# Optimization experiments

Hardware: AMD Instinct MI355X
Metric: run time of the kernel (lower is better)

## Reference

```python
import jax, jax.numpy as jnp
import numpy as np

EPS = 1e-5

def mvn(x):
    # per-(N,C) spatial mean/std normalization; torch .var is unbiased (ddof=1)
    mean = jnp.mean(x, axis=(2, 3), keepdims=True)
    var = jnp.var(x, axis=(2, 3), ddof=1, keepdims=True)
    return (x - mean) / jnp.sqrt(var + EPS)

def conv1x1(x, w, b):
    # w: [O, C] (1x1 conv collapsed), x: [B, C, H, W]
    return jnp.einsum('bchw,oc->bohw', x, w) + b[None, :, None, None]

def conv3x3(x, w, b):
    # w: [O, I, 3, 3], VALID padding (snet uses padding=0)
    y = jax.lax.conv_general_dilated(x, w, (1, 1), 'VALID',
                                     dimension_numbers=('NCHW', 'OIHW', 'NCHW'))
    return y + b[None, :, None, None]

def safe_cbrt(x):
    # pow(relu(x), 1/3) with safe gradient at 0 (forward identical)
    pos = x > 0
    return jnp.where(pos, jnp.power(jnp.where(pos, x, 1.0), 1.0 / 3.0), 0.0)

def _forward(content, style, wf_san, bf_san, wg_san, bg_san, wh_san, bh_san,
             wf_mcc, bf_mcc, wg_mcc, bg_mcc, w_fc, b_fc, w_out, b_out,
             wc1, bc1, wc2, bc2, wc3, bc3, ws1, bs1, ws2, bs2, ws3, bs3,
             w_unc, b_unc):
    B, C, H, W = content.shape
    cn = mvn(content)
    sn = mvn(style)

    # --- MCC branch: channel correlation statistic of style ---
    F_Fc = conv1x1(cn, wf_mcc, bf_mcc)                      # [B,C,H,W]
    g = conv1x1(sn, wg_mcc, bg_mcc).reshape(B, C, H * W)    # [B,C,HW]
    FC_S = jnp.sum(g * g, axis=-1) / jnp.sum(g, axis=-1)    # [B,C]
    FC_S = FC_S @ w_fc.T + b_fc                             # Linear
    part1 = F_Fc * FC_S[:, :, None, None]

    # --- WCT-like covariance branch (compressed 32-dim space) ---
    Fs0 = style - jnp.mean(style, axis=(2, 3), keepdims=True)  # nor_mean
    fc_ = conv1x1(jax.nn.relu(conv1x1(jax.nn.relu(conv1x1(cn, wc1, bc1)), wc2, bc2)), wc3, bc3)  # [B,32,H,W]
    fs_ = conv1x1(jax.nn.relu(conv3x3(jax.nn.relu(conv3x3(Fs0, ws1, bs1)), ws2, bs2)), ws3, bs3)  # [B,32,H-4,W-4]
    cdim = fc_.shape[1]
    fs_flat = fs_.reshape(B, cdim, -1)                       # [B,32,hw_s]
    cov = jnp.einsum('bci,bdi->bcd', fs_flat, fs_flat) / fs_flat.shape[2]  # [B,32,32]
    out = jnp.einsum('bcd,bdi->bci', cov, fc_.reshape(B, cdim, H * W)).reshape(B, cdim, H, W)
    part2 = conv1x1(out, w_unc, b_unc)                       # [B,512,H,W]

    # --- SANet-style attention branch ---
    F_s = conv1x1(cn, wf_san, bf_san).reshape(B, C, H * W)
    G_s = conv1x1(sn, wg_san, bg_san).reshape(B, C, H * W)
    H_s = conv1x1(style, wh_san, bh_san).reshape(B, C, H * W)
    S = jax.nn.softmax(jnp.einsum('bci,bcj->bij', F_s, G_s), axis=-1)  # [B,HW,HW]
    part3 = jnp.einsum('bcj,bij->bci', H_s, S).reshape(B, C, H, W)

    p = safe_cbrt(jax.nn.relu(part1 * part2 * part3))
    return conv1x1(p, w_out, b_out) + content


def setup_inputs() -> dict:
    key = jax.random.key(0)
    B, C, H, W = 16, 512, 32, 32
    s = 0.02
    shapes = {
        'content': (B, C, H, W), 'style': (B, C, H, W),
        'wf_san': (C, C), 'bf_san': (C,), 'wg_san': (C, C), 'bg_san': (C,),
        'wh_san': (C, C), 'bh_san': (C,),
        'wf_mcc': (C, C), 'bf_mcc': (C,), 'wg_mcc': (C, C), 'bg_mcc': (C,),
        'w_fc': (C, C), 'b_fc': (C,), 'w_out': (C, C), 'b_out': (C,),
        'wc1': (256, 512), 'bc1': (256,), 'wc2': (128, 256), 'bc2': (128,),
        'wc3': (32, 128), 'bc3': (32,),
        'ws1': (256, 512, 3, 3), 'bs1': (256,), 'ws2': (128, 256, 3, 3), 'bs2': (128,),
        'ws3': (32, 128), 'bs3': (32,),
        'w_unc': (512, 32), 'b_unc': (512,),
    }
    d = {}
    for i, (name, shp) in enumerate(shapes.items()):
        k = jax.random.fold_in(key, i)
        scale = 1.0 if name in ('content', 'style') else s
        d[name] = jax.random.normal(k, shp, dtype=jnp.float32) * scale
    return d


def reference(content, style, wf_san, bf_san, wg_san, bg_san, wh_san, bh_san,
              wf_mcc, bf_mcc, wg_mcc, bg_mcc, w_fc, b_fc, w_out, b_out,
              wc1, bc1, wc2, bc2, wc3, bc3, ws1, bs1, ws2, bs2, ws3, bs3,
              w_unc, b_unc):
    return _forward(content, style, wf_san, bf_san, wg_san, bg_san, wh_san, bh_san,
                    wf_mcc, bf_mcc, wg_mcc, bg_mcc, w_fc, b_fc, w_out, b_out,
                    wc1, bc1, wc2, bc2, wc3, bc3, ws1, bs1, ws2, bs2, ws3, bs3,
                    w_unc, b_unc)
```

## Files before the change

kernel.cpp:

```cpp
#include <hip/hip_runtime.h>
#include <hip/hip_bf16.h>
#include <math.h>


typedef __attribute__((ext_vector_type(8))) short short8;
typedef __attribute__((ext_vector_type(4))) float f32x4;
typedef unsigned short us;
#define MFMA16 __builtin_amdgcn_mfma_f32_16x16x32_bf16

__device__ inline float b2f(us b) { return __uint_as_float(((unsigned)b) << 16); }
__device__ inline us f2b(float f) {
    unsigned u = __float_as_uint(f);
    return (us)((u + 0x7FFFu + ((u >> 16) & 1u)) >> 16);
}

__device__ inline double blockReduceSumD(double v, double* sh) {
    int t = threadIdx.x;
    sh[t] = v; __syncthreads();
    for (int s = blockDim.x >> 1; s > 0; s >>= 1) {
        if (t < s) sh[t] += sh[t + s];
        __syncthreads();
    }
    double r = sh[0]; __syncthreads();
    return r;
}

__global__ __launch_bounds__(256) void stats_k(const float* __restrict__ X,
                                               float* __restrict__ mean,
                                               float* __restrict__ inv, int HW) {
    __shared__ double sh[256];
    int bc = blockIdx.x;
    const float* x = X + (size_t)bc * HW;
    int t = threadIdx.x;
    float v[4];
    double s = 0.0;
    #pragma unroll
    for (int r = 0; r < 4; ++r) { v[r] = x[t + r * 256]; s += (double)v[r]; }
    double tot = blockReduceSumD(s, sh);
    double ss = 0.0;
    #pragma unroll
    for (int r = 0; r < 4; ++r) ss += (double)v[r] * (double)v[r];
    double tot2 = blockReduceSumD(ss, sh);
    if (t == 0) {
        double m = tot / HW;
        double var = (tot2 - tot * tot / HW) / (HW - 1);
        mean[bc] = (float)m;
        inv[bc] = (float)(1.0 / sqrt(var + 1e-5));
    }
}

__global__ __launch_bounds__(256) void trn_k(const float* __restrict__ X,
                                             const float* __restrict__ mean,
                                             const float* __restrict__ inv,
                                             us* __restrict__ Yn, us* __restrict__ Yc,
                                             us* __restrict__ Yr, int C, int HW) {
    __shared__ us Ln[64 * 65];
    __shared__ us Lc[64 * 65];
    __shared__ us Lr[64 * 65];
    int bz = blockIdx.z, c0 = blockIdx.y * 64, h0 = blockIdx.x * 64;
    const float* Xb = X + (size_t)bz * C * HW;
    int t = threadIdx.x;
    int cl = t >> 3, h8 = (t & 7) * 8;
    #pragma unroll
    for (int half = 0; half < 2; ++half) {
        int c = cl + half * 32;
        int gc = c0 + c;
        float m = mean[bz * C + gc], iv = inv[bz * C + gc];
        const float4* s4 = (const float4*)&Xb[(size_t)gc * HW + h0 + h8];
        float4 f0 = s4[0], f1 = s4[1];
        float vv[8] = {f0.x, f0.y, f0.z, f0.w, f1.x, f1.y, f1.z, f1.w};
        #pragma unroll
        for (int i = 0; i < 8; ++i) {
            int li = c * 65 + h8 + i;
            if (Yn) Ln[li] = f2b((vv[i] - m) * iv);
            if (Yc) Lc[li] = f2b(vv[i] - m);
            if (Yr) Lr[li] = f2b(vv[i]);
        }
    }
    __syncthreads();
    int hl = t >> 3, c8 = (t & 7) * 8;
    #pragma unroll
    for (int half = 0; half < 2; ++half) {
        int hh = hl + half * 32;
        size_t off = ((size_t)bz * HW + h0 + hh) * (size_t)C + c0 + c8;
        us tmp[8];
        if (Yn) {
            #pragma unroll
            for (int i = 0; i < 8; ++i) tmp[i] = Ln[(c8 + i) * 65 + hh];
            *(uint4*)&Yn[off] = *(const uint4*)tmp;
        }
        if (Yc) {
            #pragma unroll
            for (int i = 0; i < 8; ++i) tmp[i] = Lc[(c8 + i) * 65 + hh];
            *(uint4*)&Yc[off] = *(const uint4*)tmp;
        }
        if (Yr) {
            #pragma unroll
            for (int i = 0; i < 8; ++i) tmp[i] = Lr[(c8 + i) * 65 + hh];
            *(uint4*)&Yr[off] = *(const uint4*)tmp;
        }
    }
}

template <typename TE>
__device__ inline void stage16(const TE* __restrict__ src, bool valid, us* dst) {
    us tmp[16];
    if (valid) {
        if constexpr (sizeof(TE) == 2) {
            uint4 a = ((const uint4*)src)[0], b = ((const uint4*)src)[1];
            *(uint4*)&tmp[0] = a; *(uint4*)&tmp[8] = b;
        } else {
            const float4* s4 = (const float4*)src;
            float4 f0 = s4[0], f1 = s4[1], f2 = s4[2], f3 = s4[3];
            float vv[16] = {f0.x, f0.y, f0.z, f0.w, f1.x, f1.y, f1.z, f1.w,
                            f2.x, f2.y, f2.z, f2.w, f3.x, f3.y, f3.z, f3.w};
            #pragma unroll
            for (int i = 0; i < 16; ++i) tmp[i] = f2b(vv[i]);
        }
    } else {
        #pragma unroll
        for (int i = 0; i < 16; ++i) tmp[i] = 0;
    }
    ((uint4*)dst)[0] = *(uint4*)&tmp[0];
    ((uint4*)dst)[1] = *(uint4*)&tmp[8];
}

template <typename TAel, typename TBel, typename TOUT, int OUTT>
__global__ __launch_bounds__(256) void mf2_k(const TAel* __restrict__ A, long astride, int lda,
                                             const TBel* __restrict__ B, long bstride, int ldb,
                                             const float* __restrict__ bias,
                                             TOUT* __restrict__ Y,
                                             const float* __restrict__ add_src,
                                             int K, int M, int N, int relu) {
    __shared__ us As[128][40];
    __shared__ us Bs[128][40];
    int bz = blockIdx.z;
    int mbase = blockIdx.y * 128, nbase = blockIdx.x * 128;
    const TAel* Ab = A + (size_t)bz * astride;
    const TBel* Bb = B + (size_t)bz * bstride;
    int t = threadIdx.x;
    int row = t & 127, kh = t >> 7;
    int wave = t >> 6, lane = t & 63, lm = lane & 15, q = lane >> 4;
    int mh = (wave >> 1) * 64, nh = (wave & 1) * 64;

    f32x4 acc[4][4];
    #pragma unroll
    for (int i = 0; i < 4; ++i)
        #pragma unroll
        for (int j = 0; j < 4; ++j) acc[i][j] = (f32x4){0.f, 0.f, 0.f, 0.f};

    for (int kb = 0; kb < K; kb += 32) {
        int gm = mbase + row;
        stage16(Ab + (size_t)gm * lda + kb + kh * 16, gm < M, &As[row][kh * 16]);
        int gn = nbase + row;
        stage16(Bb + (size_t)gn * ldb + kb + kh * 16, gn < N, &Bs[row][kh * 16]);
        __syncthreads();
        short8 af[4], bf[4];
        #pragma unroll
        for (int i = 0; i < 4; ++i) af[i] = *(const short8*)&As[mh + i * 16 + lm][q * 8];
        #pragma unroll
        for (int j = 0; j < 4; ++j) bf[j] = *(const short8*)&Bs[nh + j * 16 + lm][q * 8];
        #pragma unroll
        for (int i = 0; i < 4; ++i)
            #pragma unroll
            for (int j = 0; j < 4; ++j)
                acc[i][j] = MFMA16(af[i], bf[j], acc[i][j], 0, 0, 0);
        __syncthreads();
    }

    #pragma unroll
    for (int i = 0; i < 4; ++i) {
        int m0 = mbase + mh + i * 16 + q * 4;
        if (m0 >= M) continue;
        float bv[4];
        #pragma unroll
        for (int r = 0; r < 4; ++r) bv[r] = bias ? bias[m0 + r] : 0.f;
        #pragma unroll
        for (int j = 0; j < 4; ++j) {
            int n = nbase + nh + j * 16 + lm;
            if (n >= N) continue;
            float v[4];
            #pragma unroll
            for (int r = 0; r < 4; ++r) {
                float x = acc[i][j][r] + bv[r];
                if (relu) x = (x > 0.f) ? x : 0.f;
                v[r] = x;
            }
            if (OUTT == 1) {
                size_t off = ((size_t)bz * N + n) * (size_t)M + m0;
                if constexpr (sizeof(TOUT) == 2) {
                    us o4[4];
                    #pragma unroll
                    for (int r = 0; r < 4; ++r) o4[r] = f2b(v[r]);
                    *(uint2*)&Y[off] = *(const uint2*)o4;
                } else {
                    float4 f4 = make_float4(v[0], v[1], v[2], v[3]);
                    *(float4*)&Y[off] = f4;
                }
            } else {
                #pragma unroll
                for (int r = 0; r < 4; ++r) {
                    size_t off = ((size_t)bz * M + m0 + r) * (size_t)N + n;
                    float x = v[r];
                    if (add_src) x += add_src[off];
                    if constexpr (sizeof(TOUT) == 2) Y[off] = f2b(x);
                    else Y[off] = x;
                }
            }
        }
    }
}

struct SBias {
    const float* bp[10];
    int moff[10];
    unsigned relu;
};
__global__ __launch_bounds__(256) void mfs_k(const us* __restrict__ A,
                                             const us* __restrict__ B, long bstride, int ldb,
                                             us* __restrict__ Y, int ldy,
                                             SBias sb, int K, int N) {
    __shared__ us As[128][40];
    __shared__ us Bs[128][40];
    int bz = blockIdx.z;
    int mbase = blockIdx.y * 128, nbase = blockIdx.x * 128;
    const us* Bb = B + (size_t)bz * bstride;
    int t = threadIdx.x;
    int row = t & 127, kh = t >> 7;
    int wave = t >> 6, lane = t & 63, lm = lane & 15, q = lane >> 4;
    int mh = (wave >> 1) * 64, nh = (wave & 1) * 64;
    int relu = (sb.relu >> blockIdx.y) & 1;
    const float* bias = sb.bp[blockIdx.y];
    int moff = sb.moff[blockIdx.y];

    f32x4 acc[4][4];
    #pragma unroll
    for (int i = 0; i < 4; ++i)
        #pragma unroll
        for (int j = 0; j < 4; ++j) acc[i][j] = (f32x4){0.f, 0.f, 0.f, 0.f};

    for (int kb = 0; kb < K; kb += 32) {
        stage16(A + (size_t)(mbase + row) * K + kb + kh * 16, true, &As[row][kh * 16]);
        stage16(Bb + (size_t)(nbase + row) * ldb + kb + kh * 16, true, &Bs[row][kh * 16]);
        __syncthreads();
        short8 af[4], bf[4];
        #pragma unroll
        for (int i = 0; i < 4; ++i) af[i] = *(const short8*)&As[mh + i * 16 + lm][q * 8];
        #pragma unroll
        for (int j = 0; j < 4; ++j) bf[j] = *(const short8*)&Bs[nh + j * 16 + lm][q * 8];
        #pragma unroll
        for (int i = 0; i < 4; ++i)
            #pragma unroll
            for (int j = 0; j < 4; ++j)
                acc[i][j] = MFMA16(af[i], bf[j], acc[i][j], 0, 0, 0);
        __syncthreads();
    }

    #pragma unroll
    for (int i = 0; i < 4; ++i) {
        int m0 = mbase + mh + i * 16 + q * 4;
        float bv[4];
        #pragma unroll
        for (int r = 0; r < 4; ++r) bv[r] = bias[m0 - moff + r];
        #pragma unroll
        for (int j = 0; j < 4; ++j) {
            int n = nbase + nh + j * 16 + lm;
            us o4[4];
            #pragma unroll
            for (int r = 0; r < 4; ++r) {
                float x = acc[i][j][r] + bv[r];
                if (relu) x = (x > 0.f) ? x : 0.f;
                o4[r] = f2b(x);
            }
            *(uint2*)&Y[((size_t)bz * N + n) * ldy + m0] = *(const uint2*)o4;
        }
    }
}

struct CpyArg {
    const float* src[11];
    unsigned long long dstoff[11];
    int len[11];
};
__global__ __launch_bounds__(256) void wcat_k(CpyArg a, us* __restrict__ arena) {
    int seg = blockIdx.y;
    int idx = blockIdx.x * 256 + threadIdx.x;
    if (idx < a.len[seg]) arena[a.dstoff[seg] + idx] = f2b(a.src[seg][idx]);
}

__global__ __launch_bounds__(256) void reorder_wf_k(const float* __restrict__ W,
                                                    us* __restrict__ Wf, int O, int Cin) {
    int idx = blockIdx.x * 256 + threadIdx.x;
    int OT = O >> 6, KB = Cin >> 5;
    int total = OT * KB * 9 * 4 * 64;
    if (idx >= total) return;
    int lane = idx & 63;
    int f = idx >> 6;
    int i = f & 1, half = (f >> 1) & 1;
    int tf = f >> 2;
    int tap = tf % 9;
    int rest = tf / 9;
    int kb = rest % KB, ot = rest / KB;
    int o = ot * 64 + half * 32 + i * 16 + (lane & 15);
    int cb = kb * 32 + (lane >> 4) * 8;
    us v[8];
    #pragma unroll
    for (int e = 0; e < 8; ++e)
        v[e] = f2b(W[((size_t)o * Cin + cb + e) * 9 + tap]);
    *(uint4*)&Wf[(size_t)idx * 8] = *(const uint4*)v;
}

template <int PR>
__global__ __launch_bounds__(256) void conv_mf3_k(const us* __restrict__ X, long xbstride,
                                                  const us* __restrict__ Wf,
                                                  const float* __restrict__ bias,
                                                  us* __restrict__ Y, long ybstride,
                                                  int Cin, int O, int IH, int IW,
                                                  int OH, int OW) {
    __shared__ us patch[(2 * PR + 2) * 36 * 40];
    int bz = blockIdx.z;
    int obase = blockIdx.y * 64;
    int pyb = blockIdx.x * (2 * PR);
    const us* Xb = X + (size_t)bz * xbstride;
    int t = threadIdx.x;
    int wave = t >> 6, lane = t & 63, lm = lane & 15, q = lane >> 4;
    int half = wave >> 1, rw = wave & 1;
    int KB = Cin >> 5;
    const us* Wb = Wf + (size_t)(obase >> 6) * KB * 9 * 2048;

    f32x4 acc[PR][2][2];
    #pragma unroll
    for (int pr = 0; pr < PR; ++pr)
        #pragma unroll
        for (int i = 0; i < 2; ++i)
            #pragma unroll
            for (int j = 0; j < 2; ++j) acc[pr][i][j] = (f32x4){0.f, 0.f, 0.f, 0.f};

    const int ITEMS = (2 * PR + 2) * 36 * 4;
    for (int kb = 0; kb < KB; ++kb) {
        __syncthreads();
        for (int i = t; i < ITEMS; i += 256) {
            int p = i >> 2, q8 = (i & 3) * 8;
            int r = p / 36, x = p - r * 36;
            int gy = pyb + r;
            uint4 v = make_uint4(0u, 0u, 0u, 0u);
            if (x < IW && gy < IH)
                v = *(const uint4*)&Xb[((size_t)(gy * IW + x)) * Cin + kb * 32 + q8];
            *(uint4*)&patch[p * 40 + q8] = v;
        }
        __syncthreads();
        const us* Wk = Wb + (size_t)kb * 9 * 2048;
        #pragma unroll
        for (int tap = 0; tap < 9; ++tap) {
            int ky = tap / 3, kx = tap - ky * 3;
            const us* wt = Wk + tap * 2048 + half * 1024;
            short8 a0 = *(const short8*)&wt[lane * 8];
            short8 a1 = *(const short8*)&wt[512 + lane * 8];
            #pragma unroll
            for (int pr = 0; pr < PR; ++pr) {
                int prow = (pr * 2 + rw + ky) * 36;
                short8 b0 = *(const short8*)&patch[(prow + lm + kx) * 40 + q * 8];
                short8 b1 = *(const short8*)&patch[(prow + 16 + lm + kx) * 40 + q * 8];
                acc[pr][0][0] = MFMA16(a0, b0, acc[pr][0][0], 0, 0, 0);
                acc[pr][0][1] = MFMA16(a0, b1, acc[pr][0][1], 0, 0, 0);
                acc[pr][1][0] = MFMA16(a1, b0, acc[pr][1][0], 0, 0, 0);
                acc[pr][1][1] = MFMA16(a1, b1, acc[pr][1][1], 0, 0, 0);
            }
        }
    }

    us* Yb = Y + (size_t)bz * ybstride;
    #pragma unroll
    for (int pr = 0; pr < PR; ++pr) {
        int py = pyb + pr * 2 + rw;
        if (py >= OH) continue;
        #pragma unroll
        for (int i = 0; i < 2; ++i) {
            int m0 = obase + half * 32 + i * 16 + q * 4;
            #pragma unroll
            for (int j = 0; j < 2; ++j) {
                int px = j * 16 + lm;
                if (px >= OW) continue;
                us o4[4];
                #pragma unroll
                for (int r = 0; r < 4; ++r) {
                    float v = acc[pr][i][j][r] + bias[m0 + r];
                    v = (v > 0.f) ? v : 0.f;
                    o4[r] = f2b(v);
                }
                *(uint2*)&Yb[((size_t)(py * OW + px)) * O + m0] = *(const uint2*)o4;
            }
        }
    }
}

__global__ __launch_bounds__(256) void gemm_k(const float* __restrict__ W,
                                              const float* __restrict__ X,
                                              const float* __restrict__ bias,
                                              float* __restrict__ Y,
                                              int C, int O, int N) {
    int obase = blockIdx.y * 32;
    __shared__ float As[32][33];
    __shared__ float Bs[32][33];
    int t = threadIdx.x;
    int tx = t & 15, ty = t >> 4;
    float acc00 = 0, acc01 = 0, acc10 = 0, acc11 = 0;
    for (int cb = 0; cb < C; cb += 32) {
        int k = t & 31, o0 = t >> 5;
        #pragma unroll
        for (int r = 0; r < 4; ++r) {
            int ol = o0 + r * 8;
            As[k][ol] = W[(size_t)(obase + ol) * C + cb + k];
        }
        int n0 = t & 31, k0 = t >> 5;
        #pragma unroll
        for (int r = 0; r < 4; ++r) {
            int k2 = k0 + r * 8;
            Bs[k2][n0] = (n0 < N) ? X[(size_t)(cb + k2) * N + n0] : 0.f;
        }
        __syncthreads();
        #pragma unroll
        for (int k2 = 0; k2 < 32; ++k2) {
            float a0 = As[k2][ty], a1 = As[k2][ty + 16];
            float b0 = Bs[k2][tx], b1 = Bs[k2][tx + 16];
            acc00 += a0 * b0; acc01 += a0 * b1;
            acc10 += a1 * b0; acc11 += a1 * b1;
        }
        __syncthreads();
    }
    float accs[2][2] = {{acc00, acc01}, {acc10, acc11}};
    #pragma unroll
    for (int i = 0; i < 2; ++i) {
        int o = obase + ty + i * 16;
        float bv = bias[o];
        #pragma unroll
        for (int j = 0; j < 2; ++j) {
            int n = tx + j * 16;
            if (n < N) Y[(size_t)o * N + n] = accs[i][j] + bv;
        }
    }
}

__global__ __launch_bounds__(256) void fcs3_k(const us* __restrict__ g, int ldg,
                                              const float* __restrict__ bg,
                                              float* __restrict__ fcs,
                                              int B, int HW) {
    int b = blockIdx.x;
    int t = threadIdx.x;
    const us* gb = g + (size_t)b * HW * ldg + 2 * t;
    double s0 = 0.0, s1 = 0.0;
    #pragma unroll 4
    for (int hw = 0; hw < HW; ++hw) {
        unsigned u = *(const unsigned*)&gb[(size_t)hw * ldg];
        float f0 = b2f((us)(u & 0xFFFFu));
        float f1 = b2f((us)(u >> 16));
        s0 += (double)f0 * (double)f0;
        s1 += (double)f1 * (double)f1;
    }
    int c0 = 2 * t;
    fcs[(size_t)c0 * B + b] = (float)(s0 / ((double)HW * (double)bg[c0]));
    fcs[(size_t)(c0 + 1) * B + b] = (float)(s1 / ((double)HW * (double)bg[c0 + 1]));
}

__global__ __launch_bounds__(256) void softmax_k(const float* __restrict__ S,
                                                 us* __restrict__ P) {
    __shared__ float sh[256];
    size_t row = blockIdx.x;
    const float* r = S + row * 1024;
    us* po = P + row * 1024;
    int t = threadIdx.x;
    float v[4];
    float m = -INFINITY;
    #pragma unroll
    for (int i = 0; i < 4; ++i) { v[i] = r[t + i * 256]; m = fmaxf(m, v[i]); }
    sh[t] = m; __syncthreads();
    for (int s = 128; s > 0; s >>= 1) { if (t < s) sh[t] = fmaxf(sh[t], sh[t + s]); __syncthreads(); }
    m = sh[0]; __syncthreads();
    float sum = 0;
    #pragma unroll
    for (int i = 0; i < 4; ++i) { v[i] = expf(v[i] - m); sum += v[i]; }
    sh[t] = sum; __syncthreads();
    for (int s = 128; s > 0; s >>= 1) { if (t < s) sh[t] += sh[t + s]; __syncthreads(); }
    float inv = 1.f / sh[0]; __syncthreads();
    #pragma unroll
    for (int i = 0; i < 4; ++i) po[t + i * 256] = f2b(v[i] * inv);
}

__global__ __launch_bounds__(256) void cov2_k(const float* __restrict__ fs,
                                              float* __restrict__ cov, int Cd, int M) {
    __shared__ float Ls[196 * 36];
    int bb = blockIdx.x;
    int t = threadIdx.x;
    const float* p = fs + (size_t)bb * M * Cd;
    int c = t >> 3, d0 = (t & 7) * 4;
    float a0 = 0.f, a1 = 0.f, a2 = 0.f, a3 = 0.f;
    for (int ch = 0; ch < 4; ++ch) {
        __syncthreads();
        for (int i = t; i < 1568; i += 256) {
            int rowi = i >> 3, c4 = (i & 7) * 4;
            float4 v = *(const float4*)&p[(size_t)(ch * 196 + rowi) * Cd + c4];
            *(float4*)&Ls[rowi * 36 + c4] = v;
        }
        __syncthreads();
        for (int i = 0; i < 196; ++i) {
            float a = Ls[i * 36 + c];
            a0 += a * Ls[i * 36 + d0 + 0];
            a1 += a * Ls[i * 36 + d0 + 1];
            a2 += a * Ls[i * 36 + d0 + 2];
            a3 += a * Ls[i * 36 + d0 + 3];
        }
    }
    float invM = 1.f / (float)M;
    size_t base = ((size_t)bb * Cd + c) * Cd + d0;
    cov[base + 0] = a0 * invM;
    cov[base + 1] = a1 * invM;
    cov[base + 2] = a2 * invM;
    cov[base + 3] = a3 * invM;
}

__global__ __launch_bounds__(256) void fuse_k(const us* __restrict__ ffc, int ldf,
                                              const float* __restrict__ fc2t,
                                              const us* __restrict__ p2,
                                              const us* __restrict__ p3,
                                              us* __restrict__ out, int B, int C, int HW) {
    size_t idx = (size_t)blockIdx.x * 256 + threadIdx.x;
    size_t total = (size_t)B * C * HW;
    if (idx >= total) return;
    int c = (int)(idx & (size_t)(C - 1));
    size_t tok = idx >> 9;
    int b = (int)(idx / ((size_t)C * HW));
    float part1 = b2f(ffc[tok * ldf + c]) * fc2t[(size_t)c * B + b];
    float v = part1 * b2f(p2[idx]) * b2f(p3[idx]);
    v = (v > 0.f) ? v : 0.f;
    out[idx] = f2b(cbrtf(v));
}

extern "C" void kernel_launch(void* const* d_in, const int* in_sizes, int n_in,
                              void* d_out, int out_size, void* d_ws, size_t ws_size,
                              hipStream_t stream) {
    typedef const float* fp;
    fp content = (fp)d_in[0];
    fp style   = (fp)d_in[1];
    fp wf_san = (fp)d_in[2],  bf_san = (fp)d_in[3];
    fp wg_san = (fp)d_in[4],  bg_san = (fp)d_in[5];
    fp wh_san = (fp)d_in[6],  bh_san = (fp)d_in[7];
    fp wf_mcc = (fp)d_in[8],  bf_mcc = (fp)d_in[9];
    fp wg_mcc = (fp)d_in[10], bg_mcc = (fp)d_in[11];
    fp w_fc   = (fp)d_in[12], b_fc   = (fp)d_in[13];
    fp w_out  = (fp)d_in[14], b_out  = (fp)d_in[15];
    fp wc1 = (fp)d_in[16], bc1 = (fp)d_in[17];
    fp wc2 = (fp)d_in[18], bc2 = (fp)d_in[19];
    fp wc3 = (fp)d_in[20], bc3 = (fp)d_in[21];
    fp ws1 = (fp)d_in[22], bs1 = (fp)d_in[23];
    fp ws2 = (fp)d_in[24], bs2 = (fp)d_in[25];
    fp ws3 = (fp)d_in[26], bs3 = (fp)d_in[27];
    fp w_unc = (fp)d_in[28], b_unc = (fp)d_in[29];

    const int B = 16, C = 512, HW = 1024;
    const size_t NE = (size_t)B * C * HW;
    const long TOK = (long)C * HW;
    const size_t MB = 1u << 20;
    char* base = (char*)d_ws;

    float* Sbuf  = (float*)(base);
    us* cnT      = (us*)(base);
    us* snT      = (us*)(base + 16 * MB);
    us* Hco      = (us*)(base + 32 * MB);
    us* t2b      = (us*)(base);
    float* fc_c  = (float*)(base + 4 * MB);
    float* fs_c  = (float*)(base + 6 * MB);
    float* out32 = (float*)(base + 8 * MB);
    us* cnOut    = (us*)(base + 64 * MB);
    us* snOut    = (us*)(base + 104 * MB);
    us* part3b   = (us*)(base + 104 * MB);
    us* pbuf     = (us*)(base + 120 * MB);
    us* Pb       = (us*)(base + 136 * MB);
    us* part2b   = (us*)(base + 136 * MB);
    us* fs0T     = (us*)(base + 168 * MB);
    us* styleT   = (us*)(base + 184 * MB);
    us* s1       = (us*)(base + 184 * MB);
    us* s2       = (us*)(base + 192 * MB);

    char* misc = base + 200 * MB;
    us* Wr1   = (us*)(misc);
    us* Wr2   = (us*)(misc + 2359296);
    us* Wcn   = (us*)(misc + 2949120);
    us* Wsn   = (us*)(misc + 4259840);
    us* Wh    = (us*)(misc + 5308416);
    us* Wout  = (us*)(misc + 5832704);
    us* Wc2   = (us*)(misc + 6356992);
    us* Wc3   = (us*)(misc + 6422528);
    us* Ws3   = (us*)(misc + 6430720);
    us* Wunc  = (us*)(misc + 6438912);
    float* fcs   = (float*)(misc + 6471680);
    float* fc2t  = (float*)(misc + 6504448);
    float* cov   = (float*)(misc + 6537216);
    float* meanC = (float*)(misc + 6602752);
    float* invC  = (float*)(misc + 6635520);
    float* meanS = (float*)(misc + 6668288);
    float* invS  = (float*)(misc + 6701056);

    CpyArg ca;
    const float* srcs[11] = {wf_mcc, wc1, wf_san, wg_mcc, wg_san, wh_san,
                             w_out, wc2, wc3, ws3, w_unc};
    int lens[11] = {262144, 131072, 262144, 262144, 262144, 262144,
                    262144, 32768, 4096, 4096, 16384};
    unsigned long long off = 0;
    for (int i = 0; i < 11; ++i) { ca.src[i] = srcs[i]; ca.dstoff[i] = off; ca.len[i] = lens[i]; off += lens[i]; }
    wcat_k<<<dim3(1024, 11), 256, 0, stream>>>(ca, Wcn);
    reorder_wf_k<<<576, 256, 0, stream>>>(ws1, Wr1, 256, 512);
    reorder_wf_k<<<72, 256, 0, stream>>>(ws2, Wr2, 128, 256);

    stats_k<<<B * C, 256, 0, stream>>>(content, meanC, invC, HW);
    stats_k<<<B * C, 256, 0, stream>>>(style, meanS, invS, HW);
    trn_k<<<dim3(16, 8, 16), 256, 0, stream>>>(content, meanC, invC, cnT, nullptr, nullptr, C, HW);
    trn_k<<<dim3(16, 8, 16), 256, 0, stream>>>(style, meanS, invS, snT, fs0T, styleT, C, HW);

    {
        SBias sb;
        for (int y = 0; y < 4; ++y) { sb.bp[y] = bf_mcc; sb.moff[y] = 0; }
        for (int y = 4; y < 6; ++y) { sb.bp[y] = bc1; sb.moff[y] = 512; }
        for (int y = 6; y < 10; ++y) { sb.bp[y] = bf_san; sb.moff[y] = 768; }
        sb.relu = 0x030u;
        mfs_k<<<dim3(8, 10, 16), 256, 0, stream>>>(Wcn, cnT, TOK, 512, cnOut, 1280, sb, 512, 1024);
    }

    {
        SBias sb;
        for (int y = 0; y < 4; ++y) { sb.bp[y] = bg_mcc; sb.moff[y] = 0; }
        for (int y = 4; y < 8; ++y) { sb.bp[y] = bg_san; sb.moff[y] = 512; }
        for (int y = 8; y < 10; ++y) { sb.bp[y] = bg_mcc; sb.moff[y] = 0; }
        sb.relu = 0u;
        mfs_k<<<dim3(8, 8, 16), 256, 0, stream>>>(Wsn, snT, TOK, 512, snOut, 1024, sb, 512, 1024);
    }

    fcs3_k<<<B, 256, 0, stream>>>(snOut, 1024, bg_mcc, fcs, B, HW);
    gemm_k<<<dim3(1, 16, 1), 256, 0, stream>>>(w_fc, fcs, b_fc, fc2t, 512, 512, 16);

    mf2_k<us, us, float, 0><<<dim3(8, 8, 16), 256, 0, stream>>>(
        cnOut + 768, (long)1024 * 1280, 1280, snOut + 512, (long)1024 * 1024, 1024,
        nullptr, Sbuf, nullptr, 512, 1024, 1024, 0);
    softmax_k<<<B * HW, 256, 0, stream>>>(Sbuf, Pb);

    mf2_k<us, us, us, 0><<<dim3(8, 4, 16), 256, 0, stream>>>(
        Wh, 0, 512, styleT, TOK, 512, bh_san, Hco, nullptr, 512, 512, 1024, 0);

    mf2_k<us, us, us, 0><<<dim3(4, 8, 16), 256, 0, stream>>>(
        Pb, (long)1024 * 1024, 1024, Hco, TOK, 1024, nullptr, part3b, nullptr, 1024, 1024, 512, 0);

    mf2_k<us, us, us, 1><<<dim3(8, 1, 16), 256, 0, stream>>>(
        Wc2, 0, 256, cnOut + 512, (long)1024 * 1280, 1280, bc2, t2b, nullptr, 256, 128, 1024, 1);
    mf2_k<us, us, float, 1><<<dim3(8, 1, 16), 256, 0, stream>>>(
        Wc3, 0, 128, t2b, (long)1024 * 128, 128, bc3, fc_c, nullptr, 128, 32, 1024, 0);

    conv_mf3_k<2><<<dim3(8, 4, 16), 256, 0, stream>>>(fs0T, TOK, Wr1, bs1,
                                                      s1, (long)900 * 256, 512, 256, 32, 32, 30, 30);
    conv_mf3_k<1><<<dim3(14, 2, 16), 256, 0, stream>>>(s1, (long)900 * 256, Wr2, bs2,
                                                       s2, (long)784 * 128, 256, 128, 30, 30, 28, 28);
    mf2_k<us, us, float, 1><<<dim3(7, 1, 16), 256, 0, stream>>>(
        Ws3, 0, 128, s2, (long)784 * 128, 128, bs3, fs_c, nullptr, 128, 32, 784, 0);

    cov2_k<<<B, 256, 0, stream>>>(fs_c, cov, 32, 784);
    mf2_k<float, float, float, 1><<<dim3(8, 1, 16), 256, 0, stream>>>(
        cov, 1024, 32, fc_c, (long)1024 * 32, 32, nullptr, out32, nullptr, 32, 32, 1024, 0);
    mf2_k<us, float, us, 1><<<dim3(8, 4, 16), 256, 0, stream>>>(
        Wunc, 0, 32, out32, (long)1024 * 32, 32, b_unc, part2b, nullptr, 32, 512, 1024, 0);

    fuse_k<<<(unsigned)((NE + 255) / 256), 256, 0, stream>>>(
        cnOut, 1280, fc2t, part2b, part3b, pbuf, B, C, HW);

    mf2_k<us, us, float, 0><<<dim3(8, 4, 16), 256, 0, stream>>>(
        Wout, 0, 512, pbuf, TOK, 512, b_out, (float*)d_out, content, 512, 512, 1024, 0);
}
```

Measured before the change: 879.6 us.

## Double-buffer GEMM and conv LDS tiles, split fcs reduction, reorder launches

Adds two-stage shared-memory double buffering to the mf2, mfs and conv kernels, so the next K-slice is loaded while MFMAs run on the current one, with one barrier per iteration. The first 3x3 conv switches from PR=2 to PR=1, doubling its grid. The single-block-per-batch fcs reduction is split into a parallel partial-sum pass and a combine pass. Workspace buffers are relaid out so the conv branch and the Hco GEMM can be launched earlier. Doubled LDS may lower occupancy, and the global loads still go through registers, so overlap within a wave is limited.

New measurement: 769.4 us. 1.14x faster.

```diff
diff --git a/kernel.cpp b/kernel.cpp
--- a/kernel.cpp
+++ b/kernel.cpp
@@ -132,8 +132,8 @@
                                              TOUT* __restrict__ Y,
                                              const float* __restrict__ add_src,
                                              int K, int M, int N, int relu) {
-    __shared__ us As[128][40];
-    __shared__ us Bs[128][40];
+    __shared__ us As[2][128][40];
+    __shared__ us Bs[2][128][40];
     int bz = blockIdx.z;
     int mbase = blockIdx.y * 128, nbase = blockIdx.x * 128;
     const TAel* Ab = A + (size_t)bz * astride;
@@ -142,6 +142,13 @@
     int row = t & 127, kh = t >> 7;
     int wave = t >> 6, lane = t & 63, lm = lane & 15, q = lane >> 4;
     int mh = (wave >> 1) * 64, nh = (wave & 1) * 64;
+    int gm = mbase + row, gn = nbase + row;
+    bool vm = gm < M, vn = gn < N;
+
+    auto stage = [&](int buf, int kb) {
+        stage16(Ab + (size_t)gm * lda + kb + kh * 16, vm, &As[buf][row][kh * 16]);
+        stage16(Bb + (size_t)gn * ldb + kb + kh * 16, vn, &Bs[buf][row][kh * 16]);
+    };
 
     f32x4 acc[4][4];
     #pragma unroll
@@ -149,23 +156,23 @@
         #pragma unroll
         for (int j = 0; j < 4; ++j) acc[i][j] = (f32x4){0.f, 0.f, 0.f, 0.f};
 
+    stage(0, 0);
+    __syncthreads();
+    int cur = 0;
     for (int kb = 0; kb < K; kb += 32) {
-        int gm = mbase + row;
-        stage16(Ab + (size_t)gm * lda + kb + kh * 16, gm < M, &As[row][kh * 16]);
-        int gn = nbase + row;
-        stage16(Bb + (size_t)gn * ldb + kb + kh * 16, gn < N, &Bs[row][kh * 16]);
-        __syncthreads();
+        if (kb + 32 < K) stage(cur ^ 1, kb + 32);
         short8 af[4], bf[4];
         #pragma unroll
-        for (int i = 0; i < 4; ++i) af[i] = *(const short8*)&As[mh + i * 16 + lm][q * 8];
-        #pragma unroll
-        for (int j = 0; j < 4; ++j) bf[j] = *(const short8*)&Bs[nh + j * 16 + lm][q * 8];
+        for (int i = 0; i < 4; ++i) af[i] = *(const short8*)&As[cur][mh + i * 16 + lm][q * 8];
+        #pragma unroll
+        for (int j = 0; j < 4; ++j) bf[j] = *(const short8*)&Bs[cur][nh + j * 16 + lm][q * 8];
         #pragma unroll
         for (int i = 0; i < 4; ++i)
             #pragma unroll
             for (int j = 0; j < 4; ++j)
                 acc[i][j] = MFMA16(af[i], bf[j], acc[i][j], 0, 0, 0);
         __syncthreads();
+        cur ^= 1;
     }
 
     #pragma unroll
@@ -220,8 +227,8 @@
                                              const us* __restrict__ B, long bstride, int ldb,
                                              us* __restrict__ Y, int ldy,
                                              SBias sb, int K, int N) {
-    __shared__ us As[128][40];
-    __shared__ us Bs[128][40];
+    __shared__ us As[2][128][40];
+    __shared__ us Bs[2][128][40];
     int bz = blockIdx.z;
     int mbase = blockIdx.y * 128, nbase = blockIdx.x * 128;
     const us* Bb = B + (size_t)bz * bstride;
@@ -233,27 +240,34 @@
     const float* bias = sb.bp[blockIdx.y];
     int moff = sb.moff[blockIdx.y];
 
+    auto stage = [&](int buf, int kb) {
+        stage16(A + (size_t)(mbase + row) * K + kb + kh * 16, true, &As[buf][row][kh * 16]);
+        stage16(Bb + (size_t)(nbase + row) * ldb + kb + kh * 16, true, &Bs[buf][row][kh * 16]);
+    };
+
     f32x4 acc[4][4];
     #pragma unroll
     for (int i = 0; i < 4; ++i)
         #pragma unroll
         for (int j = 0; j < 4; ++j) acc[i][j] = (f32x4){0.f, 0.f, 0.f, 0.f};
 
+    stage(0, 0);
+    __syncthreads();
+    int cur = 0;
     for (int kb = 0; kb < K; kb += 32) {
-        stage16(A + (size_t)(mbase + row) * K + kb + kh * 16, true, &As[row][kh * 16]);
-        stage16(Bb + (size_t)(nbase + row) * ldb + kb + kh * 16, true, &Bs[row][kh * 16]);
-        __syncthreads();
+        if (kb + 32 < K) stage(cur ^ 1, kb + 32);
         short8 af[4], bf[4];
         #pragma unroll
-        for (int i = 0; i < 4; ++i) af[i] = *(const short8*)&As[mh + i * 16 + lm][q * 8];
-        #pragma unroll
-        for (int j = 0; j < 4; ++j) bf[j] = *(const short8*)&Bs[nh + j * 16 + lm][q * 8];
+        for (int i = 0; i < 4; ++i) af[i] = *(const short8*)&As[cur][mh + i * 16 + lm][q * 8];
+        #pragma unroll
+        for (int j = 0; j < 4; ++j) bf[j] = *(const short8*)&Bs[cur][nh + j * 16 + lm][q * 8];
         #pragma unroll
         for (int i = 0; i < 4; ++i)
             #pragma unroll
             for (int j = 0; j < 4; ++j)
                 acc[i][j] = MFMA16(af[i], bf[j], acc[i][j], 0, 0, 0);
         __syncthreads();
+        cur ^= 1;
     }
 
     #pragma unroll
@@ -311,13 +325,28 @@
 }
 
 template <int PR>
-__global__ __launch_bounds__(256) void conv_mf3_k(const us* __restrict__ X, long xbstride,
+__device__ inline void stage_patch(const us* __restrict__ Xb, us* __restrict__ dst,
+                                   int pyb, int kb, int Cin, int IH, int IW, int t) {
+    const int ITEMS = (2 * PR + 2) * 36 * 4;
+    for (int i = t; i < ITEMS; i += 256) {
+        int p = i >> 2, q8 = (i & 3) * 8;
+        int r = p / 36, x = p - r * 36;
+        int gy = pyb + r;
+        uint4 v = make_uint4(0u, 0u, 0u, 0u);
+        if (x < IW && gy < IH)
+            v = *(const uint4*)&Xb[((size_t)(gy * IW + x)) * Cin + kb * 32 + q8];
+        *(uint4*)&dst[p * 40 + q8] = v;
+    }
+}
+
+template <int PR>
+__global__ __launch_bounds__(256) void conv_mf4_k(const us* __restrict__ X, long xbstride,
                                                   const us* __restrict__ Wf,
                                                   const float* __restrict__ bias,
                                                   us* __restrict__ Y, long ybstride,
                                                   int Cin, int O, int IH, int IW,
                                                   int OH, int OW) {
-    __shared__ us patch[(2 * PR + 2) * 36 * 40];
+    __shared__ us patch[2][(2 * PR + 2) * 36 * 40];
     int bz = blockIdx.z;
     int obase = blockIdx.y * 64;
     int pyb = blockIdx.x * (2 * PR);
@@ -336,19 +365,11 @@
             #pragma unroll
             for (int j = 0; j < 2; ++j) acc[pr][i][j] = (f32x4){0.f, 0.f, 0.f, 0.f};
 
-    const int ITEMS = (2 * PR + 2) * 36 * 4;
+    stage_patch<PR>(Xb, patch[0], pyb, 0, Cin, IH, IW, t);
+    __syncthreads();
+    int cur = 0;
     for (int kb = 0; kb < KB; ++kb) {
-        __syncthreads();
-        for (int i = t; i < ITEMS; i += 256) {
-            int p = i >> 2, q8 = (i & 3) * 8;
-            int r = p / 36, x = p - r * 36;
-            int gy = pyb + r;
-            uint4 v = make_uint4(0u, 0u, 0u, 0u);
-            if (x < IW && gy < IH)
-                v = *(const uint4*)&Xb[((size_t)(gy * IW + x)) * Cin + kb * 32 + q8];
-            *(uint4*)&patch[p * 40 + q8] = v;
-        }
-        __syncthreads();
+        if (kb + 1 < KB) stage_patch<PR>(Xb, patch[cur ^ 1], pyb, kb + 1, Cin, IH, IW, t);
         const us* Wk = Wb + (size_t)kb * 9 * 2048;
         #pragma unroll
         for (int tap = 0; tap < 9; ++tap) {
@@ -359,14 +380,16 @@
             #pragma unroll
             for (int pr = 0; pr < PR; ++pr) {
                 int prow = (pr * 2 + rw + ky) * 36;
-                short8 b0 = *(const short8*)&patch[(prow + lm + kx) * 40 + q * 8];
-                short8 b1 = *(const short8*)&patch[(prow + 16 + lm + kx) * 40 + q * 8];
+                short8 b0 = *(const short8*)&patch[cur][(prow + lm + kx) * 40 + q * 8];
+                short8 b1 = *(const short8*)&patch[cur][(prow + 16 + lm + kx) * 40 + q * 8];
                 acc[pr][0][0] = MFMA16(a0, b0, acc[pr][0][0], 0, 0, 0);
                 acc[pr][0][1] = MFMA16(a0, b1, acc[pr][0][1], 0, 0, 0);
                 acc[pr][1][0] = MFMA16(a1, b0, acc[pr][1][0], 0, 0, 0);
                 acc[pr][1][1] = MFMA16(a1, b1, acc[pr][1][1], 0, 0, 0);
             }
         }
+        __syncthreads();
+        cur ^= 1;
     }
 
     us* Yb = Y + (size_t)bz * ybstride;
@@ -441,21 +464,34 @@
     }
 }
 
-__global__ __launch_bounds__(256) void fcs3_k(const us* __restrict__ g, int ldg,
-                                              const float* __restrict__ bg,
-                                              float* __restrict__ fcs,
-                                              int B, int HW) {
-    int b = blockIdx.x;
-    int t = threadIdx.x;
-    const us* gb = g + (size_t)b * HW * ldg + 2 * t;
+__global__ __launch_bounds__(256) void fcs3a_k(const us* __restrict__ g, int ldg,
+                                               float* __restrict__ pa, int HW) {
+    int b = blockIdx.x, j = blockIdx.y;
+    int t = threadIdx.x;
+    const us* gb = g + ((size_t)b * HW + (size_t)j * 128) * ldg + 2 * t;
     double s0 = 0.0, s1 = 0.0;
     #pragma unroll 4
-    for (int hw = 0; hw < HW; ++hw) {
+    for (int hw = 0; hw < 128; ++hw) {
         unsigned u = *(const unsigned*)&gb[(size_t)hw * ldg];
         float f0 = b2f((us)(u & 0xFFFFu));
         float f1 = b2f((us)(u >> 16));
         s0 += (double)f0 * (double)f0;
         s1 += (double)f1 * (double)f1;
+    }
+    float2 w = make_float2((float)s0, (float)s1);
+    *(float2*)&pa[((size_t)b * 8 + j) * 512 + 2 * t] = w;
+}
+
+__global__ __launch_bounds__(256) void fcs3b_k(const float* __restrict__ pa,
+                                               const float* __restrict__ bg,
+                                               float* __restrict__ fcs, int B, int HW) {
+    int b = blockIdx.x;
+    int t = threadIdx.x;
+    double s0 = 0.0, s1 = 0.0;
+    #pragma unroll
+    for (int j = 0; j < 8; ++j) {
+        float2 w = *(const float2*)&pa[((size_t)b * 8 + j) * 512 + 2 * t];
+        s0 += (double)w.x; s1 += (double)w.y;
     }
     int c0 = 2 * t;
     fcs[(size_t)c0 * B + b] = (float)(s0 / ((double)HW * (double)bg[c0]));
@@ -562,43 +598,45 @@
     const size_t MB = 1u << 20;
     char* base = (char*)d_ws;
 
-    float* Sbuf  = (float*)(base);
     us* cnT      = (us*)(base);
     us* snT      = (us*)(base + 16 * MB);
-    us* Hco      = (us*)(base + 32 * MB);
-    us* t2b      = (us*)(base);
-    float* fc_c  = (float*)(base + 4 * MB);
-    float* fs_c  = (float*)(base + 6 * MB);
-    float* out32 = (float*)(base + 8 * MB);
+    us* fs0T     = (us*)(base + 32 * MB);
+    us* s1       = (us*)(base + 48 * MB);
+    us* s2       = (us*)(base + 56 * MB);
+    float* fs_c  = (float*)(base + 60 * MB);
+    float* Sbuf  = (float*)(base);
     us* cnOut    = (us*)(base + 64 * MB);
     us* snOut    = (us*)(base + 104 * MB);
     us* part3b   = (us*)(base + 104 * MB);
-    us* pbuf     = (us*)(base + 120 * MB);
+    us* part2b   = (us*)(base + 120 * MB);
     us* Pb       = (us*)(base + 136 * MB);
-    us* part2b   = (us*)(base + 136 * MB);
-    us* fs0T     = (us*)(base + 168 * MB);
-    us* styleT   = (us*)(base + 184 * MB);
-    us* s1       = (us*)(base + 184 * MB);
-    us* s2       = (us*)(base + 192 * MB);
+    us* t2b      = (us*)(base + 136 * MB);
+    float* fc_c  = (float*)(base + 140 * MB);
+    float* out32 = (float*)(base + 142 * MB);
+    us* pbuf     = (us*)(base + 144 * MB);
+    us* styleT   = (us*)(base + 168 * MB);
+    us* Hco      = (us*)(base + 184 * MB);
 
     char* misc = base + 200 * MB;
     us* Wr1   = (us*)(misc);
     us* Wr2   = (us*)(misc + 2359296);
-    us* Wcn   = (us*)(misc + 2949120);
-    us* Wsn   = (us*)(misc + 4259840);
-    us* Wh    = (us*)(misc + 5308416);
-    us* Wout  = (us*)(misc + 5832704);
-    us* Wc2   = (us*)(misc + 6356992);
-    us* Wc3   = (us*)(misc + 6422528);
-    us* Ws3   = (us*)(misc + 6430720);
-    us* Wunc  = (us*)(misc + 6438912);
-    float* fcs   = (float*)(misc + 6471680);
-    float* fc2t  = (float*)(misc + 6504448);
-    float* cov   = (float*)(misc + 6537216);
-    float* meanC = (float*)(misc + 6602752);
-    float* invC  = (float*)(misc + 6635520);
-    float* meanS = (float*)(misc + 6668288);
-    float* invS  = (float*)(misc + 6701056);
+    us* arena = (us*)(misc + 2949120);
+    us* Wcn   = arena;
+    us* Wsn   = arena + 655360;
+    us* Wh    = arena + 1179648;
+    us* Wout  = arena + 1441792;
+    us* Wc2   = arena + 1703936;
+    us* Wc3   = arena + 1736704;
+    us* Ws3   = arena + 1740800;
+    us* Wunc  = arena + 1744896;
+    float* pa    = (float*)(misc + 6471680);
+    float* fcs   = (float*)(misc + 6733824);
+    float* fc2t  = (float*)(misc + 6766592);
+    float* cov   = (float*)(misc + 6799360);
+    float* meanC = (float*)(misc + 6864896);
+    float* invC  = (float*)(misc + 6897664);
+    float* meanS = (float*)(misc + 6930432);
+    float* invS  = (float*)(misc + 6963200);
 
     CpyArg ca;
     const float* srcs[11] = {wf_mcc, wc1, wf_san, wg_mcc, wg_san, wh_san,
@@ -607,7 +645,7 @@
                     262144, 32768, 4096, 4096, 16384};
     unsigned long long off = 0;
     for (int i = 0; i < 11; ++i) { ca.src[i] = srcs[i]; ca.dstoff[i] = off; ca.len[i] = lens[i]; off += lens[i]; }
-    wcat_k<<<dim3(1024, 11), 256, 0, stream>>>(ca, Wcn);
+    wcat_k<<<dim3(1024, 11), 256, 0, stream>>>(ca, arena);
     reorder_wf_k<<<576, 256, 0, stream>>>(ws1, Wr1, 256, 512);
     reorder_wf_k<<<72, 256, 0, stream>>>(ws2, Wr2, 128, 256);
 
@@ -615,6 +653,14 @@
     stats_k<<<B * C, 256, 0, stream>>>(style, meanS, invS, HW);
     trn_k<<<dim3(16, 8, 16), 256, 0, stream>>>(content, meanC, invC, cnT, nullptr, nullptr, C, HW);
     trn_k<<<dim3(16, 8, 16), 256, 0, stream>>>(style, meanS, invS, snT, fs0T, styleT, C, HW);
+
+    conv_mf4_k<1><<<dim3(15, 4, 16), 256, 0, stream>>>(fs0T, TOK, Wr1, bs1,
+                                                       s1, (long)900 * 256, 512, 256, 32, 32, 30, 30);
+    conv_mf4_k<1><<<dim3(14, 2, 16), 256, 0, stream>>>(s1, (long)900 * 256, Wr2, bs2,
+                                                       s2, (long)784 * 128, 256, 128, 30, 30, 28, 28);
+    mf2_k<us, us, float, 1><<<dim3(7, 1, 16), 256, 0, stream>>>(
+        Ws3, 0, 128, s2, (long)784 * 128, 128, bs3, fs_c, nullptr, 128, 32, 784, 0);
+    cov2_k<<<B, 256, 0, stream>>>(fs_c, cov, 32, 784);
 
     {
         SBias sb;
@@ -634,17 +680,18 @@
         mfs_k<<<dim3(8, 8, 16), 256, 0, stream>>>(Wsn, snT, TOK, 512, snOut, 1024, sb, 512, 1024);
     }
 
-    fcs3_k<<<B, 256, 0, stream>>>(snOut, 1024, bg_mcc, fcs, B, HW);
+    fcs3a_k<<<dim3(B, 8), 256, 0, stream>>>(snOut, 1024, pa, HW);
+    fcs3b_k<<<B, 256, 0, stream>>>(pa, bg_mcc, fcs, B, HW);
     gemm_k<<<dim3(1, 16, 1), 256, 0, stream>>>(w_fc, fcs, b_fc, fc2t, 512, 512, 16);
+
+    mf2_k<us, us, us, 0><<<dim3(8, 4, 16), 256, 0, stream>>>(
+        Wh, 0, 512, styleT, TOK, 512, bh_san, Hco, nullptr, 512, 512, 1024, 0);
 
     mf2_k<us, us, float, 0><<<dim3(8, 8, 16), 256, 0, stream>>>(
         cnOut + 768, (long)1024 * 1280, 1280, snOut + 512, (long)1024 * 1024, 1024,
         nullptr, Sbuf, nullptr, 512, 1024, 1024, 0);
     softmax_k<<<B * HW, 256, 0, stream>>>(Sbuf, Pb);
 
-    mf2_k<us, us, us, 0><<<dim3(8, 4, 16), 256, 0, stream>>>(
-        Wh, 0, 512, styleT, TOK, 512, bh_san, Hco, nullptr, 512, 512, 1024, 0);
-
     mf2_k<us, us, us, 0><<<dim3(4, 8, 16), 256, 0, stream>>>(
         Pb, (long)1024 * 1024, 1024, Hco, TOK, 1024, nullptr, part3b, nullptr, 1024, 1024, 512, 0);
 
@@ -653,14 +700,6 @@
     mf2_k<us, us, float, 1><<<dim3(8, 1, 16), 256, 0, stream>>>(
         Wc3, 0, 128, t2b, (long)1024 * 128, 128, bc3, fc_c, nullptr, 128, 32, 1024, 0);
 
-    conv_mf3_k<2><<<dim3(8, 4, 16), 256, 0, stream>>>(fs0T, TOK, Wr1, bs1,
-                                                      s1, (long)900 * 256, 512, 256, 32, 32, 30, 30);
-    conv_mf3_k<1><<<dim3(14, 2, 16), 256, 0, stream>>>(s1, (long)900 * 256, Wr2, bs2,
-                                                       s2, (long)784 * 128, 256, 128, 30, 30, 28, 28);
-    mf2_k<us, us, float, 1><<<dim3(7, 1, 16), 256, 0, stream>>>(
-        Ws3, 0, 128, s2, (long)784 * 128, 128, bs3, fs_c, nullptr, 128, 32, 784, 0);
-
-    cov2_k<<<B, 256, 0, stream>>>(fs_c, cov, 32, 784);
     mf2_k<float, float, float, 1><<<dim3(8, 1, 16), 256, 0, stream>>>(
         cov, 1024, 32, fc_c, (long)1024 * 32, 32, nullptr, out32, nullptr, 32, 32, 1024, 0);
     mf2_k<us, float, us, 1><<<dim3(8, 4, 16), 256, 0, stream>>>(
```
